# Kernel optimization log

Hardware: AMD Instinct MI355X
Metric: run time of the kernel (lower is better)

## Reference

```python
import jax, jax.numpy as jnp
import numpy as np

EPS = 0.5      # sinkhorn eps used by assign_batch_sinkhorn
NITERS = 15    # sinkhorn iterations used by assign_batch_sinkhorn


def pairwise_dists(features, centroids):
    # ||f - c|| via the expansion ||f||^2 + ||c||^2 - 2 f.c (avoids the
    # [B, nc, D] intermediate the naive broadcast would materialize).
    f2 = jnp.sum(features * features, axis=-1)          # [B]
    c2 = jnp.sum(centroids * centroids, axis=-1)        # [K]
    d2 = f2[:, None] + c2[None, :] - 2.0 * features @ centroids.T  # [B, K]
    return jnp.sqrt(jnp.maximum(d2, 0.0))


def sinkhorn(scores, eps=EPS, niters=NITERS):
    # Faithful to the torch sinkhorn(): Q = exp(scores/eps).T, normalize
    # columns (sum over K), then alternate row/column scalings.
    Q = jnp.exp(scores / eps).T                          # [K, B]
    Q = Q / jnp.sum(Q, axis=0, keepdims=True)
    K, B = Q.shape
    r = jnp.ones((K,), Q.dtype) / K
    c = jnp.ones((B,), Q.dtype) / B

    def body(_, Q):
        Q = Q * (r / jnp.sum(Q, axis=1))[:, None]
        Q = Q * (c / jnp.sum(Q, axis=0))[None, :]
        return Q

    Q = jax.lax.fori_loop(0, niters, body, Q)
    return (Q / jnp.sum(Q, axis=0, keepdims=True)).T     # [B, K]


def setup_inputs() -> dict:
    key = jax.random.key(0)
    kf, kc = jax.random.split(key)
    B, K, D = 16384, 2048, 1000
    # 0.1 scale keeps dists ~O(5) so exp(-dists/eps) stays in fp32 range
    # (unit-randn 1000-dim features give dists ~45 -> exp underflow).
    features = 0.1 * jax.random.normal(kf, (B, D), dtype=jnp.float32)
    centroids = 0.1 * jax.random.normal(kc, (K, D), dtype=jnp.float32)
    return {"features": features, "centroids": centroids}


def reference(features, centroids):
    B, K = features.shape[0], centroids.shape[0]
    dists = pairwise_dists(features, centroids)          # [B, K]

    # assign_batch_sinkhorn (soft assignments computed under no_grad)
    soft = jax.lax.stop_gradient(sinkhorn(-dists))       # [B, K]
    batch_assignments = jnp.argmin(soft, axis=1)         # [B] (as in source)
    soft_counts = jnp.sum(soft, axis=0)                  # [K]
    cluster_loss = jnp.mean(
        jnp.take_along_axis(dists, batch_assignments[:, None], axis=1))

    # the per-element python count loops, as fused scatter-adds
    cluster_counts = jnp.zeros((K,), jnp.int32).at[batch_assignments].add(1)
    raw_assign = jnp.argmin(dists, axis=1)
    raw_counts = jnp.zeros((K,), jnp.int32).at[raw_assign].add(1)

    return cluster_loss, batch_assignments, soft_counts, cluster_counts, raw_counts
```

## Files before the change

kernel.cpp:

```cpp
#include <hip/hip_runtime.h>

typedef __attribute__((ext_vector_type(8))) short bf16x8;
typedef __attribute__((ext_vector_type(4))) float f32x4;

#define NB 16384
#define NK 2048
#define ND 1000
#define KP 1024
#define NCHK 1024

__device__ float  g_dist[(size_t)NB * NK];
__device__ ushort g_E[(size_t)NB * NK];
__device__ ushort g_Fh[(size_t)NB * KP], g_Fl[(size_t)NB * KP];
__device__ ushort g_Ch[(size_t)NK * KP], g_Cl[(size_t)NK * KP];
__device__ float  g_u[NK], g_c2[NK], g_scnt[NK];
__device__ float  g_f2[NB], g_bd[NB];
__device__ float  g_part[(size_t)NCHK * NK];
__device__ int    g_cc[NK], g_rc[NK];

typedef const __attribute__((address_space(1))) void gvoid_t;
typedef __attribute__((address_space(3))) void lvoid_t;

union h16 { ushort u; _Float16 h; };

__device__ __forceinline__ ushort bf16_rne(float x){
    uint u = __float_as_uint(x);
    uint lsb = (u >> 16) & 1u;
    u += 0x7fffu + lsb;
    return (ushort)(u >> 16);
}
__device__ __forceinline__ float bf16_to_f(ushort h){
    return __uint_as_float(((uint)h) << 16);
}

template<int WHICH>
__global__ __launch_bounds__(256) void cn_prep(const float* __restrict__ X){
    ushort* __restrict__ H = WHICH ? g_Ch : g_Fh;
    ushort* __restrict__ L = WHICH ? g_Cl : g_Fl;
    float*  __restrict__ sq = WHICH ? g_c2 : g_f2;
    const int row = blockIdx.x, t = threadIdx.x;
    const int lane = t & 63, wid = t >> 6;
    float4 x = make_float4(0.f,0.f,0.f,0.f);
    if (t < 250) x = *(const float4*)(X + (size_t)row * ND + 4 * t);
    double s = (double)x.x*x.x + (double)x.y*x.y + (double)x.z*x.z + (double)x.w*x.w;
    ushort4 h4, l4;
#pragma unroll
    for (int c = 0; c < 4; ++c){
        float xc = (&x.x)[c];
        ushort h = bf16_rne(xc);
        (&h4.x)[c] = h;
        (&l4.x)[c] = bf16_rne(xc - bf16_to_f(h));
    }
    const int base = (t >> 3) << 5;
    const int grp  = (t >> 1) & 3;
    const int pos  = base + ((grp ^ ((row >> 1) & 3)) << 3) + ((4 * t) & 7);
    *(ushort4*)&H[(size_t)row * KP + pos] = h4;
    *(ushort4*)&L[(size_t)row * KP + pos] = l4;

    __shared__ double pr[4];
    for (int off = 32; off; off >>= 1) s += __shfl_xor(s, off);
    if (lane == 0) pr[wid] = s;
    __syncthreads();
    if (t == 0) sq[row] = (float)(pr[0] + pr[1] + pr[2] + pr[3]);
}

__global__ __launch_bounds__(256) void cn_gemm_dist(){
    __shared__ __attribute__((aligned(16))) ushort Ah[128 * 32];
    __shared__ __attribute__((aligned(16))) ushort Al[128 * 32];
    __shared__ __attribute__((aligned(16))) ushort Bh[128 * 32];
    __shared__ __attribute__((aligned(16))) ushort Bl[128 * 32];

    const int tid = threadIdx.x;
    const int lane = tid & 63, wid = tid >> 6;
    const int wr = wid >> 1, wc = wid & 1;
    const int brow0 = blockIdx.y * 128, bcol0 = blockIdx.x * 128;

    f32x4 acc[4][4];
#pragma unroll
    for (int m = 0; m < 4; ++m)
#pragma unroll
        for (int n = 0; n < 4; ++n) acc[m][n] = (f32x4){0.f,0.f,0.f,0.f};

    const int lrow = lane >> 2;
    const int lcol = (lane & 3) * 8;

    for (int step = 0; step < 32; ++step){
        const int k0 = step * 32;
#pragma unroll
        for (int i = 0; i < 2; ++i){
            const int ch = wid * 2 + i;
            const int ldso = ch * 512;
            const size_t ga = ((size_t)(brow0 + ch * 16 + lrow)) * KP + k0 + lcol;
            const size_t gb = ((size_t)(bcol0 + ch * 16 + lrow)) * KP + k0 + lcol;
            __builtin_amdgcn_global_load_lds((gvoid_t*)(g_Fh + ga), (lvoid_t*)(Ah + ldso), 16, 0, 0);
            __builtin_amdgcn_global_load_lds((gvoid_t*)(g_Fl + ga), (lvoid_t*)(Al + ldso), 16, 0, 0);
            __builtin_amdgcn_global_load_lds((gvoid_t*)(g_Ch + gb), (lvoid_t*)(Bh + ldso), 16, 0, 0);
            __builtin_amdgcn_global_load_lds((gvoid_t*)(g_Cl + gb), (lvoid_t*)(Bl + ldso), 16, 0, 0);
        }
        __syncthreads();

        const int arow = wr * 64 + (lane & 15);
        const int brow = wc * 64 + (lane & 15);
        const int kof  = (((lane >> 4) ^ ((lane >> 1) & 3)) * 8);
        bf16x8 afh[4], afl[4], bfh[4], bfl[4];
#pragma unroll
        for (int m = 0; m < 4; ++m){
            afh[m] = *(const bf16x8*)&Ah[(arow + m * 16) * 32 + kof];
            afl[m] = *(const bf16x8*)&Al[(arow + m * 16) * 32 + kof];
        }
#pragma unroll
        for (int n = 0; n < 4; ++n){
            bfh[n] = *(const bf16x8*)&Bh[(brow + n * 16) * 32 + kof];
            bfl[n] = *(const bf16x8*)&Bl[(brow + n * 16) * 32 + kof];
        }
#pragma unroll
        for (int m = 0; m < 4; ++m)
#pragma unroll
            for (int n = 0; n < 4; ++n){
                acc[m][n] = __builtin_amdgcn_mfma_f32_16x16x32_bf16(afh[m], bfh[n], acc[m][n], 0, 0, 0);
                acc[m][n] = __builtin_amdgcn_mfma_f32_16x16x32_bf16(afh[m], bfl[n], acc[m][n], 0, 0, 0);
                acc[m][n] = __builtin_amdgcn_mfma_f32_16x16x32_bf16(afl[m], bfh[n], acc[m][n], 0, 0, 0);
            }
        __syncthreads();
    }

#pragma unroll
    for (int m = 0; m < 4; ++m){
        int rowb = brow0 + wr * 64 + m * 16 + (lane >> 4) * 4;
#pragma unroll
        for (int n = 0; n < 4; ++n){
            int col = bcol0 + wc * 64 + n * 16 + (lane & 15);
            float c2v = g_c2[col];
#pragma unroll
            for (int j = 0; j < 4; ++j){
                float d2 = g_f2[rowb + j] + c2v - 2.0f * acc[m][n][j];
                float d  = sqrtf(fmaxf(d2, 0.0f));
                size_t idx = (size_t)(rowb + j) * NK + col;
                g_dist[idx] = d;
                h16 cv; cv.h = (_Float16)(__expf(-2.0f * d) * 8192.0f);
                g_E[idx] = cv.u;
            }
        }
    }
}

template<int MODE>
__global__ __launch_bounds__(256) void cn_sweep(float* __restrict__ outba){
    __shared__ float4 sred[3][8][64];
    const int lane = threadIdx.x & 63, wid = threadIdx.x >> 6;
    const int row0 = (blockIdx.x * 4 + wid) * 4;
    const float cst = (MODE == 0) ? 1.0f : (1.0f / (float)NB);

    float4 uu[8];
    float4 ak[8];
    if (MODE >= 1){
#pragma unroll
        for (int j = 0; j < 8; ++j)
            uu[j] = *(const float4*)&g_u[4 * lane + 256 * j];
    }
    if (MODE == 3){
#pragma unroll
        for (int j = 0; j < 8; ++j)
#pragma unroll
            for (int c = 0; c < 4; ++c)
                (&ak[j].x)[c] = (float)log((double)(&uu[j].x)[c] * (double)NK);
    }

    float4 S[8];
#pragma unroll
    for (int j = 0; j < 8; ++j) S[j] = make_float4(0.f,0.f,0.f,0.f);

    for (int r = 0; r < 4; ++r){
        const int b = row0 + r;
        float4 ev[8];
        float4 dv[8];
        float tsum = 0.f;
        if (MODE <= 1){
            const ushort* er = g_E + (size_t)b * NK + 4 * lane;
#pragma unroll
            for (int j = 0; j < 8; ++j){
                ushort4 q4 = *(const ushort4*)(er + 256 * j);
                float4 e4;
#pragma unroll
                for (int c = 0; c < 4; ++c){
                    h16 cv; cv.u = (&q4.x)[c];
                    float e = (float)cv.h;
                    (&e4.x)[c] = e;
                    tsum += (MODE == 1) ? e * (&uu[j].x)[c] : e;
                }
                ev[j] = e4;
            }
        } else {
            const float* dr = g_dist + (size_t)b * NK + 4 * lane;
#pragma unroll
            for (int j = 0; j < 8; ++j){
                float4 d4 = *(const float4*)(dr + 256 * j);
                float4 e4;
#pragma unroll
                for (int c = 0; c < 4; ++c){
                    float e = __expf(-2.0f * (&d4.x)[c]);
                    (&e4.x)[c] = e;
                    tsum += e * (&uu[j].x)[c];
                }
                ev[j] = e4;
                if (MODE == 3) dv[j] = d4;
            }
        }
#pragma unroll
        for (int off = 32; off; off >>= 1) tsum += __shfl_xor(tsum, off);
        const float v = cst / tsum;
#pragma unroll
        for (int j = 0; j < 8; ++j){
#pragma unroll
            for (int c = 0; c < 4; ++c)
                (&S[j].x)[c] += (&ev[j].x)[c] * v;
        }

        if (MODE == 3){
            double bestT = -1.0e300; int bi = 0; float bd = 0.f;
            float rbest = 3.4e38f;   int ri = 0;
#pragma unroll
            for (int j = 0; j < 8; ++j){
#pragma unroll
                for (int c = 0; c < 4; ++c){
                    int k = 256 * j + 4 * lane + c;
                    float d = (&dv[j].x)[c];
                    double t = 2.0 * (double)d - (double)(&ak[j].x)[c];
                    if (t > bestT){ bestT = t; bi = k; bd = d; }
                    if (d < rbest){ rbest = d; ri = k; }
                }
            }
            for (int off = 32; off; off >>= 1){
                double oT = __shfl_xor(bestT, off);
                int    oi = __shfl_xor(bi, off);
                float  od = __shfl_xor(bd, off);
                if (oT > bestT || (oT == bestT && oi < bi)){ bestT = oT; bi = oi; bd = od; }
                float orb = __shfl_xor(rbest, off);
                int   ori = __shfl_xor(ri, off);
                if (orb < rbest || (orb == rbest && ori < ri)){ rbest = orb; ri = ori; }
            }
            if (lane == 0){
                outba[b] = (float)bi;
                g_bd[b] = bd;
                atomicAdd(&g_cc[bi], 1);
                atomicAdd(&g_rc[ri], 1);
            }
        }
    }

    if (wid > 0){
#pragma unroll
        for (int j = 0; j < 8; ++j) sred[wid - 1][j][lane] = S[j];
    }
    __syncthreads();
    if (wid == 0){
#pragma unroll
        for (int w = 0; w < 3; ++w)
#pragma unroll
            for (int j = 0; j < 8; ++j){
                float4 o = sred[w][j][lane];
                S[j].x += o.x; S[j].y += o.y; S[j].z += o.z; S[j].w += o.w;
            }
#pragma unroll
        for (int j = 0; j < 8; ++j)
            *(float4*)&g_part[(size_t)blockIdx.x * NK + 4 * lane + 256 * j] = S[j];
    }
}

__global__ __launch_bounds__(256) void cn_red(int mode){
    __shared__ double red[4][64];
    const int lane = threadIdx.x & 63, q = threadIdx.x >> 6;
    const int k = blockIdx.x * 64 + lane;
    double s = 0.0;
    for (int ch = q * 256; ch < q * 256 + 256; ++ch)
        s += (double)g_part[(size_t)ch * NK + k];
    red[q][lane] = s;
    __syncthreads();
    if (q == 0){
        double tot = red[0][lane] + red[1][lane] + red[2][lane] + red[3][lane];
        if (mode == 0) g_u[k] = (float)((1.0 / (double)NK) / tot);
        else           g_scnt[k] = (float)((double)NB * (double)g_u[k] * tot);
    }
}

__global__ __launch_bounds__(256) void cn_zero(){
    int i = blockIdx.x * 256 + threadIdx.x;
    if (i < NK){ g_cc[i] = 0; g_rc[i] = 0; }
}

__global__ __launch_bounds__(256) void cn_finalize(float* __restrict__ out){
    int i = blockIdx.x * 256 + threadIdx.x;
    if (i < NK){
        out[1 + NB + i]            = g_scnt[i];
        out[1 + NB + NK + i]       = (float)g_cc[i];
        out[1 + NB + 2 * NK + i]   = (float)g_rc[i];
    }
    if (blockIdx.x == 0){
        __shared__ double red[4];
        int lane = threadIdx.x & 63, wid = threadIdx.x >> 6;
        double s = 0.0;
        for (int b = threadIdx.x; b < NB; b += 256) s += (double)g_bd[b];
        for (int off = 32; off; off >>= 1) s += __shfl_xor(s, off);
        if (lane == 0) red[wid] = s;
        __syncthreads();
        if (threadIdx.x == 0){
            double tot = red[0] + red[1] + red[2] + red[3];
            out[0] = (float)(tot / (double)NB);
        }
    }
}

extern "C" void kernel_launch(void* const* d_in, const int* in_sizes, int n_in,
                              void* d_out, int out_size, void* d_ws, size_t ws_size,
                              hipStream_t stream){
    const float* F  = (const float*)d_in[0];
    const float* Cn = (const float*)d_in[1];
    float* out = (float*)d_out;
    (void)d_ws; (void)ws_size;

    cn_prep<0><<<NB, 256, 0, stream>>>(F);
    cn_prep<1><<<NK, 256, 0, stream>>>(Cn);
    cn_zero<<<NK / 256, 256, 0, stream>>>();

    dim3 gg(NK / 128, NB / 128);
    cn_gemm_dist<<<gg, 256, 0, stream>>>();

    cn_sweep<0><<<NCHK, 256, 0, stream>>>(nullptr);
    cn_red<<<NK / 64, 256, 0, stream>>>(0);

    for (int it = 1; it <= 9; ++it){
        cn_sweep<1><<<NCHK, 256, 0, stream>>>(nullptr);
        cn_red<<<NK / 64, 256, 0, stream>>>(0);
    }
    for (int it = 10; it <= 14; ++it){
        cn_sweep<2><<<NCHK, 256, 0, stream>>>(nullptr);
        cn_red<<<NK / 64, 256, 0, stream>>>(0);
    }

    cn_sweep<3><<<NCHK, 256, 0, stream>>>(out + 1);
    cn_red<<<NK / 64, 256, 0, stream>>>(1);

    cn_finalize<<<NK / 256, 256, 0, stream>>>(out);
}
```

Baseline: 775.5 us.

## Fuse Sinkhorn sweeps and reductions into one persistent kernel with grid barriers

Replaces the 16 sweep launches, 16 reduction launches, and the zero/finalize kernels with a single persistent kernel of 256 blocks. The blocks synchronise through a software grid barrier built on an atomic counter and generation word. Each block now handles 64 rows per iteration, so the partial-sum buffer shrinks from 1024 to 256 chunks and the reduction is done in-kernel. The aim is to remove launch overhead and shorten the partial reduction. The cost is far fewer blocks (256 on a 256-CU part) for streaming the big E/dist matrices, plus reliance on all blocks being co-resident for the barrier to avoid deadlock.

```diff
diff --git a/kernel.cpp b/kernel.cpp
--- a/kernel.cpp
+++ b/kernel.cpp
@@ -7,16 +7,17 @@
 #define NK 2048
 #define ND 1000
 #define KP 1024
-#define NCHK 1024
+#define PBLK 256
 
 __device__ float  g_dist[(size_t)NB * NK];
 __device__ ushort g_E[(size_t)NB * NK];
 __device__ ushort g_Fh[(size_t)NB * KP], g_Fl[(size_t)NB * KP];
 __device__ ushort g_Ch[(size_t)NK * KP], g_Cl[(size_t)NK * KP];
-__device__ float  g_u[NK], g_c2[NK], g_scnt[NK];
+__device__ float  g_u[NK], g_c2[NK];
 __device__ float  g_f2[NB], g_bd[NB];
-__device__ float  g_part[(size_t)NCHK * NK];
+__device__ float  g_part[(size_t)PBLK * NK];
 __device__ int    g_cc[NK], g_rc[NK];
+__device__ uint   g_bar_count, g_bar_gen;
 
 typedef const __attribute__((address_space(1))) void gvoid_t;
 typedef __attribute__((address_space(3))) void lvoid_t;
@@ -31,6 +32,31 @@
 }
 __device__ __forceinline__ float bf16_to_f(ushort h){
     return __uint_as_float(((uint)h) << 16);
+}
+
+__device__ __forceinline__ float aload(const float* p){
+    return __hip_atomic_load(p, __ATOMIC_RELAXED, __HIP_MEMORY_SCOPE_AGENT);
+}
+__device__ __forceinline__ void astore(float* p, float v){
+    __hip_atomic_store(p, v, __ATOMIC_RELAXED, __HIP_MEMORY_SCOPE_AGENT);
+}
+
+__device__ __forceinline__ void grid_sync(){
+    __syncthreads();
+    if (threadIdx.x == 0){
+        __threadfence();
+        uint gen = __hip_atomic_load(&g_bar_gen, __ATOMIC_RELAXED, __HIP_MEMORY_SCOPE_AGENT);
+        uint prev = __hip_atomic_fetch_add(&g_bar_count, 1u, __ATOMIC_ACQ_REL, __HIP_MEMORY_SCOPE_AGENT);
+        if (prev == gridDim.x - 1){
+            __hip_atomic_store(&g_bar_count, 0u, __ATOMIC_RELAXED, __HIP_MEMORY_SCOPE_AGENT);
+            __hip_atomic_fetch_add(&g_bar_gen, 1u, __ATOMIC_ACQ_REL, __HIP_MEMORY_SCOPE_AGENT);
+        } else {
+            while (__hip_atomic_load(&g_bar_gen, __ATOMIC_ACQUIRE, __HIP_MEMORY_SCOPE_AGENT) == gen)
+                __builtin_amdgcn_s_sleep(2);
+        }
+        __threadfence();
+    }
+    __syncthreads();
 }
 
 template<int WHICH>
@@ -144,169 +170,167 @@
     }
 }
 
-template<int MODE>
-__global__ __launch_bounds__(256) void cn_sweep(float* __restrict__ outba){
+__global__ __launch_bounds__(256) void cn_sinkhorn(float* __restrict__ out){
+    const int lane = threadIdx.x & 63, wid = threadIdx.x >> 6;
+    const int gtid = blockIdx.x * 256 + (int)threadIdx.x;
+    const int b0 = blockIdx.x * 64 + wid * 16;
+
+    if (gtid < NK){ g_cc[gtid] = 0; g_rc[gtid] = 0; }
+
     __shared__ float4 sred[3][8][64];
-    const int lane = threadIdx.x & 63, wid = threadIdx.x >> 6;
-    const int row0 = (blockIdx.x * 4 + wid) * 4;
-    const float cst = (MODE == 0) ? 1.0f : (1.0f / (float)NB);
-
-    float4 uu[8];
-    float4 ak[8];
-    if (MODE >= 1){
-#pragma unroll
-        for (int j = 0; j < 8; ++j)
-            uu[j] = *(const float4*)&g_u[4 * lane + 256 * j];
-    }
-    if (MODE == 3){
-#pragma unroll
-        for (int j = 0; j < 8; ++j)
-#pragma unroll
-            for (int c = 0; c < 4; ++c)
-                (&ak[j].x)[c] = (float)log((double)(&uu[j].x)[c] * (double)NK);
-    }
-
-    float4 S[8];
-#pragma unroll
-    for (int j = 0; j < 8; ++j) S[j] = make_float4(0.f,0.f,0.f,0.f);
-
-    for (int r = 0; r < 4; ++r){
-        const int b = row0 + r;
-        float4 ev[8];
-        float4 dv[8];
-        float tsum = 0.f;
-        if (MODE <= 1){
-            const ushort* er = g_E + (size_t)b * NK + 4 * lane;
+    __shared__ double lred[4];
+
+    for (int it = 0; it <= 15; ++it){
+        const int useW = (it >= 1);
+        const int f16  = (it <= 9);
+        const int fin  = (it == 15);
+        const float cst = (it == 0) ? 1.0f : (1.0f / (float)NB);
+
+        float4 uu[8], ak[8];
+        if (useW){
+#pragma unroll
+            for (int j = 0; j < 8; ++j)
+#pragma unroll
+                for (int c = 0; c < 4; ++c)
+                    (&uu[j].x)[c] = aload(&g_u[4 * lane + 256 * j + c]);
+        }
+        if (fin){
+#pragma unroll
+            for (int j = 0; j < 8; ++j)
+#pragma unroll
+                for (int c = 0; c < 4; ++c)
+                    (&ak[j].x)[c] = (float)log((double)(&uu[j].x)[c] * (double)NK);
+        }
+
+        float4 S[8];
+#pragma unroll
+        for (int j = 0; j < 8; ++j) S[j] = make_float4(0.f,0.f,0.f,0.f);
+
+        for (int r = 0; r < 16; ++r){
+            const int b = b0 + r;
+            float4 ev[8], dv[8];
+            float tsum = 0.f;
+            if (f16){
+                const ushort* er = g_E + (size_t)b * NK + 4 * lane;
+#pragma unroll
+                for (int j = 0; j < 8; ++j){
+                    ushort4 q4 = *(const ushort4*)(er + 256 * j);
+                    float4 e4;
+#pragma unroll
+                    for (int c = 0; c < 4; ++c){
+                        h16 cv; cv.u = (&q4.x)[c];
+                        float e = (float)cv.h;
+                        (&e4.x)[c] = e;
+                        tsum += useW ? e * (&uu[j].x)[c] : e;
+                    }
+                    ev[j] = e4;
+                }
+            } else {
+                const float* dr = g_dist + (size_t)b * NK + 4 * lane;
+#pragma unroll
+                for (int j = 0; j < 8; ++j){
+                    float4 d4 = *(const float4*)(dr + 256 * j);
+                    float4 e4;
+#pragma unroll
+                    for (int c = 0; c < 4; ++c){
+                        float e = __expf(-2.0f * (&d4.x)[c]);
+                        (&e4.x)[c] = e;
+                        tsum += e * (&uu[j].x)[c];
+                    }
+                    ev[j] = e4;
+                    if (fin) dv[j] = d4;
+                }
+            }
+#pragma unroll
+            for (int off = 32; off; off >>= 1) tsum += __shfl_xor(tsum, off);
+            const float v = cst / tsum;
 #pragma unroll
             for (int j = 0; j < 8; ++j){
-                ushort4 q4 = *(const ushort4*)(er + 256 * j);
-                float4 e4;
-#pragma unroll
-                for (int c = 0; c < 4; ++c){
-                    h16 cv; cv.u = (&q4.x)[c];
-                    float e = (float)cv.h;
-                    (&e4.x)[c] = e;
-                    tsum += (MODE == 1) ? e * (&uu[j].x)[c] : e;
-                }
-                ev[j] = e4;
-            }
-        } else {
-            const float* dr = g_dist + (size_t)b * NK + 4 * lane;
-#pragma unroll
-            for (int j = 0; j < 8; ++j){
-                float4 d4 = *(const float4*)(dr + 256 * j);
-                float4 e4;
-#pragma unroll
-                for (int c = 0; c < 4; ++c){
-                    float e = __expf(-2.0f * (&d4.x)[c]);
-                    (&e4.x)[c] = e;
-                    tsum += e * (&uu[j].x)[c];
-                }
-                ev[j] = e4;
-                if (MODE == 3) dv[j] = d4;
-            }
-        }
-#pragma unroll
-        for (int off = 32; off; off >>= 1) tsum += __shfl_xor(tsum, off);
-        const float v = cst / tsum;
-#pragma unroll
-        for (int j = 0; j < 8; ++j){
-#pragma unroll
-            for (int c = 0; c < 4; ++c)
-                (&S[j].x)[c] += (&ev[j].x)[c] * v;
-        }
-
-        if (MODE == 3){
-            double bestT = -1.0e300; int bi = 0; float bd = 0.f;
-            float rbest = 3.4e38f;   int ri = 0;
-#pragma unroll
-            for (int j = 0; j < 8; ++j){
-#pragma unroll
-                for (int c = 0; c < 4; ++c){
-                    int k = 256 * j + 4 * lane + c;
-                    float d = (&dv[j].x)[c];
-                    double t = 2.0 * (double)d - (double)(&ak[j].x)[c];
-                    if (t > bestT){ bestT = t; bi = k; bd = d; }
-                    if (d < rbest){ rbest = d; ri = k; }
-                }
-            }
-            for (int off = 32; off; off >>= 1){
-                double oT = __shfl_xor(bestT, off);
-                int    oi = __shfl_xor(bi, off);
-                float  od = __shfl_xor(bd, off);
-                if (oT > bestT || (oT == bestT && oi < bi)){ bestT = oT; bi = oi; bd = od; }
-                float orb = __shfl_xor(rbest, off);
-                int   ori = __shfl_xor(ri, off);
-                if (orb < rbest || (orb == rbest && ori < ri)){ rbest = orb; ri = ori; }
-            }
-            if (lane == 0){
-                outba[b] = (float)bi;
-                g_bd[b] = bd;
-                atomicAdd(&g_cc[bi], 1);
-                atomicAdd(&g_rc[ri], 1);
-            }
-        }
-    }
-
-    if (wid > 0){
-#pragma unroll
-        for (int j = 0; j < 8; ++j) sred[wid - 1][j][lane] = S[j];
-    }
-    __syncthreads();
-    if (wid == 0){
-#pragma unroll
-        for (int w = 0; w < 3; ++w)
-#pragma unroll
-            for (int j = 0; j < 8; ++j){
-                float4 o = sred[w][j][lane];
-                S[j].x += o.x; S[j].y += o.y; S[j].z += o.z; S[j].w += o.w;
-            }
-#pragma unroll
-        for (int j = 0; j < 8; ++j)
-            *(float4*)&g_part[(size_t)blockIdx.x * NK + 4 * lane + 256 * j] = S[j];
-    }
-}
-
-__global__ __launch_bounds__(256) void cn_red(int mode){
-    __shared__ double red[4][64];
-    const int lane = threadIdx.x & 63, q = threadIdx.x >> 6;
-    const int k = blockIdx.x * 64 + lane;
-    double s = 0.0;
-    for (int ch = q * 256; ch < q * 256 + 256; ++ch)
-        s += (double)g_part[(size_t)ch * NK + k];
-    red[q][lane] = s;
-    __syncthreads();
-    if (q == 0){
-        double tot = red[0][lane] + red[1][lane] + red[2][lane] + red[3][lane];
-        if (mode == 0) g_u[k] = (float)((1.0 / (double)NK) / tot);
-        else           g_scnt[k] = (float)((double)NB * (double)g_u[k] * tot);
-    }
-}
-
-__global__ __launch_bounds__(256) void cn_zero(){
-    int i = blockIdx.x * 256 + threadIdx.x;
-    if (i < NK){ g_cc[i] = 0; g_rc[i] = 0; }
-}
-
-__global__ __launch_bounds__(256) void cn_finalize(float* __restrict__ out){
-    int i = blockIdx.x * 256 + threadIdx.x;
-    if (i < NK){
-        out[1 + NB + i]            = g_scnt[i];
-        out[1 + NB + NK + i]       = (float)g_cc[i];
-        out[1 + NB + 2 * NK + i]   = (float)g_rc[i];
+                S[j].x += ev[j].x * v; S[j].y += ev[j].y * v;
+                S[j].z += ev[j].z * v; S[j].w += ev[j].w * v;
+            }
+
+            if (fin){
+                double bestT = -1.0e300; int bi = 0; float bd = 0.f;
+                float rbest = 3.4e38f;   int ri = 0;
+#pragma unroll
+                for (int j = 0; j < 8; ++j){
+#pragma unroll
+                    for (int c = 0; c < 4; ++c){
+                        int k = 256 * j + 4 * lane + c;
+                        float d = (&dv[j].x)[c];
+                        double t = 2.0 * (double)d - (double)(&ak[j].x)[c];
+                        if (t > bestT){ bestT = t; bi = k; bd = d; }
+                        if (d < rbest){ rbest = d; ri = k; }
+                    }
+                }
+                for (int off = 32; off; off >>= 1){
+                    double oT = __shfl_xor(bestT, off);
+                    int    oi = __shfl_xor(bi, off);
+                    float  od = __shfl_xor(bd, off);
+                    if (oT > bestT || (oT == bestT && oi < bi)){ bestT = oT; bi = oi; bd = od; }
+                    float orb = __shfl_xor(rbest, off);
+                    int   ori = __shfl_xor(ri, off);
+                    if (orb < rbest || (orb == rbest && ori < ri)){ rbest = orb; ri = ori; }
+                }
+                if (lane == 0){
+                    out[1 + b] = (float)bi;
+                    astore(&g_bd[b], bd);
+                    atomicAdd(&g_cc[bi], 1);
+                    atomicAdd(&g_rc[ri], 1);
+                }
+            }
+        }
+
+        if (wid > 0){
+#pragma unroll
+            for (int j = 0; j < 8; ++j) sred[wid - 1][j][lane] = S[j];
+        }
+        __syncthreads();
+        if (wid == 0){
+#pragma unroll
+            for (int w = 0; w < 3; ++w)
+#pragma unroll
+                for (int j = 0; j < 8; ++j){
+                    float4 o = sred[w][j][lane];
+                    S[j].x += o.x; S[j].y += o.y; S[j].z += o.z; S[j].w += o.w;
+                }
+#pragma unroll
+            for (int j = 0; j < 8; ++j)
+#pragma unroll
+                for (int c = 0; c < 4; ++c)
+                    astore(&g_part[(size_t)blockIdx.x * NK + 4 * lane + 256 * j + c], (&S[j].x)[c]);
+        }
+        grid_sync();
+
+        {
+            const int k = gtid >> 5, sub = gtid & 31;
+            double s = 0.0;
+#pragma unroll
+            for (int i = 0; i < 8; ++i)
+                s += (double)aload(&g_part[(size_t)(sub * 8 + i) * NK + k]);
+            s += __shfl_xor(s, 16); s += __shfl_xor(s, 8);
+            s += __shfl_xor(s, 4);  s += __shfl_xor(s, 2);  s += __shfl_xor(s, 1);
+            if (sub == 0){
+                if (!fin) astore(&g_u[k], (float)((1.0 / (double)NK) / s));
+                else      out[1 + NB + k] = (float)((double)NB * (double)aload(&g_u[k]) * s);
+            }
+        }
+        grid_sync();
+    }
+
+    if (gtid < NK){
+        out[1 + NB + NK + gtid]     = (float)g_cc[gtid];
+        out[1 + NB + 2 * NK + gtid] = (float)g_rc[gtid];
     }
     if (blockIdx.x == 0){
-        __shared__ double red[4];
-        int lane = threadIdx.x & 63, wid = threadIdx.x >> 6;
         double s = 0.0;
-        for (int b = threadIdx.x; b < NB; b += 256) s += (double)g_bd[b];
+        for (int b = threadIdx.x; b < NB; b += 256) s += (double)aload(&g_bd[b]);
         for (int off = 32; off; off >>= 1) s += __shfl_xor(s, off);
-        if (lane == 0) red[wid] = s;
+        if (lane == 0) lred[wid] = s;
         __syncthreads();
-        if (threadIdx.x == 0){
-            double tot = red[0] + red[1] + red[2] + red[3];
-            out[0] = (float)(tot / (double)NB);
-        }
+        if (threadIdx.x == 0)
+            out[0] = (float)((lred[0] + lred[1] + lred[2] + lred[3]) / (double)NB);
     }
 }
 
@@ -320,25 +344,9 @@
 
     cn_prep<0><<<NB, 256, 0, stream>>>(F);
     cn_prep<1><<<NK, 256, 0, stream>>>(Cn);
-    cn_zero<<<NK / 256, 256, 0, stream>>>();
 
     dim3 gg(NK / 128, NB / 128);
     cn_gemm_dist<<<gg, 256, 0, stream>>>();
 
-    cn_sweep<0><<<NCHK, 256, 0, stream>>>(nullptr);
-    cn_red<<<NK / 64, 256, 0, stream>>>(0);
-
-    for (int it = 1; it <= 9; ++it){
-        cn_sweep<1><<<NCHK, 256, 0, stream>>>(nullptr);
-        cn_red<<<NK / 64, 256, 0, stream>>>(0);
-    }
-    for (int it = 10; it <= 14; ++it){
-        cn_sweep<2><<<NCHK, 256, 0, stream>>>(nullptr);
-        cn_red<<<NK / 64, 256, 0, stream>>>(0);
-    }
-
-    cn_sweep<3><<<NCHK, 256, 0, stream>>>(out + 1);
-    cn_red<<<NK / 64, 256, 0, stream>>>(1);
-
-    cn_finalize<<<NK / 256, 256, 0, stream>>>(out);
-}
+    cn_sinkhorn<<<PBLK, 256, 0, stream>>>(out);
+}
```

Result: slower. 2.194 ms (+182.9%).
